# Kernel tuning notes

Measured on AMD Instinct MI355X. Metric: run time of the kernel, lower is better.

Reference implementation:

```python
import jax, jax.numpy as jnp
import numpy as np

N, E, D, C = 100000, 3200000, 256, 47


def _l2norm(x):
    n = jnp.sqrt(jnp.sum(x * x, axis=-1, keepdims=True))
    return x / jnp.maximum(n, 1e-12)


def setup_inputs() -> dict:
    key = jax.random.key(0)
    ks = jax.random.split(key, 12)
    w = lambda k, s: jax.random.normal(k, s, dtype=jnp.float32) * 0.05
    return {
        "x": jax.random.normal(ks[0], (N, D), dtype=jnp.float32),
        "src": jax.random.randint(ks[1], (E,), 0, N, dtype=jnp.int32),
        "dst": jnp.sort(jax.random.randint(ks[2], (E,), 0, N, dtype=jnp.int32)),
        "W_pre": w(ks[3], (D, D)), "b_pre": jnp.zeros((D,), jnp.float32),
        "Wl1": w(ks[4], (D, D)), "bl1": jnp.zeros((D,), jnp.float32),
        "Wr1": w(ks[5], (D, D)),
        "Wl2": w(ks[6], (D, D)), "bl2": jnp.zeros((D,), jnp.float32),
        "Wr2": w(ks[7], (D, D)),
        "W_jk": w(ks[8], (D, D)), "b_jk": jnp.zeros((D,), jnp.float32),
        "W_post": w(ks[9], (C, D)), "b_post": jnp.zeros((C,), jnp.float32),
    }


def _sage_conv(x, src, dst, Wl, bl, Wr):
    # aggr='add': m_i = sum_{j in N(i)} x_j  (SpMM as gather + segment_sum)
    m = jax.ops.segment_sum(x[src], dst, num_segments=N)
    out = m @ Wl.T + bl + x @ Wr.T  # lin_l(aggr) + lin_r(root)
    return _l2norm(out)            # SAGEConv normalize=True


def reference(x, src, dst, W_pre, b_pre, Wl1, bl1, Wr1, Wl2, bl2, Wr2,
              W_jk, b_jk, W_post, b_post):
    # pre-MLP (1 layer) + classifier activation; dropout=0, batch_norm off
    h = jax.nn.relu(x @ W_pre.T + b_pre)
    h = _l2norm(h)  # self.normalize
    # GraphSAGE, jk='last': act+dropout after every conv, then jk lin
    h = jax.nn.relu(_sage_conv(h, src, dst, Wl1, bl1, Wr1))
    h = jax.nn.relu(_sage_conv(h, src, dst, Wl2, bl2, Wr2))
    h = h @ W_jk.T + b_jk
    # post: act + post-MLP (1 layer)
    h = jax.nn.relu(h)
    h = h @ W_post.T + b_post
    return jax.nn.log_softmax(h, axis=-1)
```

## Files before the change

### kernel.cpp

```cpp
#include <hip/hip_runtime.h>
#include <stdint.h>

#define DEV __device__ __forceinline__

typedef __attribute__((ext_vector_type(8))) short bh8;
typedef __attribute__((ext_vector_type(4))) float f4;
typedef __attribute__((ext_vector_type(2))) uint32_t u32x2;
#define LDS_AS __attribute__((address_space(3)))
#define GLB_AS __attribute__((address_space(1)))

DEV unsigned short f2bf(float f) {
    union { float f; uint32_t u; } c; c.f = f;
    uint32_t u = c.u;
    uint32_t r = (u + 0x7fffu + ((u >> 16) & 1u)) >> 16;
    return (unsigned short)r;
}
DEV float bf2f(unsigned short h) {
    union { uint32_t u; float f; } c; c.u = ((uint32_t)h) << 16;
    return c.f;
}

DEV uint8_t f2fp8(float v) {
    const float vs = v * 256.f;
    union { float f; uint32_t u; } c; c.f = vs;
    const uint32_t u = c.u + 0x7ffffu + ((c.u >> 20) & 1u);
    const uint32_t f8 = (u >> 20) - 960u;
    return (vs < 0.015625f) ? (uint8_t)0 : (uint8_t)f8;
}
DEV float fp8w(uint32_t x) { union { uint32_t u; float f; } c; c.u = x; return c.f; }
DEV unsigned short fp82bf(uint32_t f) {
    return f ? (unsigned short)((f << 4) + 0x3800u) : (unsigned short)0;
}

DEV void gload16(const void* g, void* l) {
    __builtin_amdgcn_global_load_lds((const GLB_AS uint32_t*)g, (LDS_AS uint32_t*)l, 16, 0, 0);
}

__global__ __launch_bounds__(256) void prep_kernel(
    const float* __restrict__ w0, const float* __restrict__ w1, const float* __restrict__ w2,
    const float* __restrict__ w3, const float* __restrict__ w4, const float* __restrict__ w5,
    unsigned short* __restrict__ wbBase,
    const int* __restrict__ dst, int* __restrict__ rp, int N, int E) {
    const int b = blockIdx.x;
    if (b < 384) {
        const int wi = b >> 6;
        const int i = (b & 63) * 256 + threadIdx.x;
        const float* s = wi == 0 ? w0 : wi == 1 ? w1 : wi == 2 ? w2 : wi == 3 ? w3 : wi == 4 ? w4 : w5;
        const float4 v = ((const float4*)s)[i];
        ushort4 o; o.x = f2bf(v.x); o.y = f2bf(v.y); o.z = f2bf(v.z); o.w = f2bf(v.w);
        ((ushort4*)(wbBase + (size_t)wi * 65536))[i] = o;
    } else {
        const int i = (b - 384) * 256 + threadIdx.x;
        if (i <= N) {
            int lo = 0, hi = E;
            while (lo < hi) { int mid = (lo + hi) >> 1; if (dst[mid] < i) lo = mid + 1; else hi = mid; }
            rp[i] = lo;
        }
    }
}

__global__ __launch_bounds__(256) void agg_fp8_kernel(const uint32_t* __restrict__ h32,
                                                      const int* __restrict__ src,
                                                      const int* __restrict__ rp,
                                                      unsigned short* __restrict__ mout, int nNodes) {
    const int node = blockIdx.x * 4 + (threadIdx.x >> 6);
    if (node >= nNodes) return;
    const int lane = threadIdx.x & 63;
    const int beg = __builtin_amdgcn_readfirstlane(rp[node]);
    const int end = __builtin_amdgcn_readfirstlane(rp[node + 1]);
    float a0 = 0.f, a1 = 0.f, a2 = 0.f, a3 = 0.f;
    int e = beg;
    for (; e + 8 <= end; e += 8) {
        int s[8];
#pragma unroll
        for (int i = 0; i < 8; i++) s[i] = src[e + i];
        uint32_t w[8];
#pragma unroll
        for (int i = 0; i < 8; i++) w[i] = h32[(size_t)s[i] * 64 + lane];
#pragma unroll
        for (int i = 0; i < 8; i++) {
            a0 += fp8w((w[i] << 20) & 0x07f00000u);
            a1 += fp8w((w[i] << 12) & 0x07f00000u);
            a2 += fp8w((w[i] << 4)  & 0x07f00000u);
            a3 += fp8w((w[i] >> 4)  & 0x07f00000u);
        }
    }
    for (; e < end; ++e) {
        const uint32_t w = h32[(size_t)src[e] * 64 + lane];
        a0 += fp8w((w << 20) & 0x07f00000u);
        a1 += fp8w((w << 12) & 0x07f00000u);
        a2 += fp8w((w << 4)  & 0x07f00000u);
        a3 += fp8w((w >> 4)  & 0x07f00000u);
    }
    const float sc = 0x1p112f;
    u32x2 o;
    o.x = (uint32_t)f2bf(a0 * sc) | ((uint32_t)f2bf(a1 * sc) << 16);
    o.y = (uint32_t)f2bf(a2 * sc) | ((uint32_t)f2bf(a3 * sc) << 16);
    __builtin_nontemporal_store(o, (u32x2*)&mout[(size_t)node * 256 + (size_t)lane * 4]);
}

__global__ __launch_bounds__(256) void agg_kernel(const unsigned short* __restrict__ h,
                                                  const int* __restrict__ src,
                                                  const int* __restrict__ rp,
                                                  unsigned short* __restrict__ mout, int nNodes) {
    const int node = blockIdx.x * 4 + (threadIdx.x >> 6);
    if (node >= nNodes) return;
    const int lane = threadIdx.x & 63;
    const size_t fo = (size_t)lane * 4;
    const int beg = __builtin_amdgcn_readfirstlane(rp[node]);
    const int end = __builtin_amdgcn_readfirstlane(rp[node + 1]);
    float a0 = 0.f, a1 = 0.f, a2 = 0.f, a3 = 0.f;
    int e = beg;
    for (; e + 4 <= end; e += 4) {
        const int s0 = src[e], s1 = src[e+1], s2 = src[e+2], s3 = src[e+3];
        ushort4 v0 = *(const ushort4*)&h[(size_t)s0 * 256 + fo];
        ushort4 v1 = *(const ushort4*)&h[(size_t)s1 * 256 + fo];
        ushort4 v2 = *(const ushort4*)&h[(size_t)s2 * 256 + fo];
        ushort4 v3 = *(const ushort4*)&h[(size_t)s3 * 256 + fo];
        a0 += bf2f(v0.x) + bf2f(v1.x) + bf2f(v2.x) + bf2f(v3.x);
        a1 += bf2f(v0.y) + bf2f(v1.y) + bf2f(v2.y) + bf2f(v3.y);
        a2 += bf2f(v0.z) + bf2f(v1.z) + bf2f(v2.z) + bf2f(v3.z);
        a3 += bf2f(v0.w) + bf2f(v1.w) + bf2f(v2.w) + bf2f(v3.w);
    }
    for (; e < end; ++e) {
        const int s = src[e];
        ushort4 v = *(const ushort4*)&h[(size_t)s * 256 + fo];
        a0 += bf2f(v.x); a1 += bf2f(v.y); a2 += bf2f(v.z); a3 += bf2f(v.w);
    }
    ushort4 o;
    o.x = f2bf(a0); o.y = f2bf(a1); o.z = f2bf(a2); o.w = f2bf(a3);
    *(ushort4*)&mout[(size_t)node * 256 + fo] = o;
}

template <int NSEG, int EPMODE, bool OUTF8, bool A0CVT, bool A1F8>
__global__ __launch_bounds__(512) void gemm_kernel(
    const void* __restrict__ A0v, const void* __restrict__ A1v,
    const unsigned short* __restrict__ B0, const unsigned short* __restrict__ B1,
    const float* __restrict__ bias, unsigned short* __restrict__ Out,
    uint8_t* __restrict__ F8, int M) {
    __shared__ unsigned short Alds[2 * 128 * 32];
    __shared__ unsigned short Blds[2 * 256 * 32];
    __shared__ float ssq_lds[8][64];

    const int t = threadIdx.x;
    const int wid = t >> 6;
    const int lane = t & 63;
    const int wr2 = wid >> 2, wc = wid & 3;
    const int l15 = lane & 15;
    const int kh = lane >> 4;
    const int rowBase = blockIdx.x * 128;

    f4 acc[4][4];
#pragma unroll
    for (int m = 0; m < 4; m++)
#pragma unroll
        for (int n = 0; n < 4; n++) acc[m][n] = f4{0.f, 0.f, 0.f, 0.f};

    const int rA = t >> 2;
    const int sSlotA = (t & 3) ^ ((rA >> 1) & 3);
    int grA = rowBase + rA; if (grA > M - 1) grA = M - 1;
    const size_t gAoff = (size_t)grA * 256 + sSlotA * 8;
    const size_t gBoff0 = (size_t)rA * 256 + sSlotA * 8;
    const size_t gBoff1 = (size_t)(128 + rA) * 256 + sSlotA * 8;

    const int nsteps = NSEG * 8;
    float4 pa0, pa1;
    uint2 pa8;

    auto LOADA = [&](int s, int buf) {
        const int k0 = (s & 7) * 32;
        const bool seg1 = (NSEG == 2 && s >= 8);
        if (!seg1) {
            if (A0CVT) {
                const float* Af = (const float*)A0v + gAoff + k0;
                pa0 = *(const float4*)Af;
                pa1 = *(const float4*)(Af + 4);
            } else {
                gload16((const unsigned short*)A0v + gAoff + k0, &Alds[buf * 4096 + wid * 512]);
            }
        } else {
            if (A1F8) {
                pa8 = *(const uint2*)&((const uint8_t*)A1v)[gAoff + k0];
            } else {
                gload16((const unsigned short*)A1v + gAoff + k0, &Alds[buf * 4096 + wid * 512]);
            }
        }
    };
    auto LOADB = [&](int s, int buf) {
        const unsigned short* Bp = (NSEG == 2 && s >= 8) ? B1 : B0;
        const int k0 = (s & 7) * 32;
        gload16(Bp + gBoff0 + k0, &Blds[buf * 8192 + wid * 512]);
        gload16(Bp + gBoff1 + k0, &Blds[buf * 8192 + 4096 + wid * 512]);
    };
    auto WRITEA = [&](int s, int buf) {
        const bool seg1 = (NSEG == 2 && s >= 8);
        if (!seg1 && A0CVT) {
            bh8 o;
            o[0] = (short)f2bf(pa0.x); o[1] = (short)f2bf(pa0.y);
            o[2] = (short)f2bf(pa0.z); o[3] = (short)f2bf(pa0.w);
            o[4] = (short)f2bf(pa1.x); o[5] = (short)f2bf(pa1.y);
            o[6] = (short)f2bf(pa1.z); o[7] = (short)f2bf(pa1.w);
            *(bh8*)&Alds[buf * 4096 + wid * 512 + lane * 8] = o;
        } else if (seg1 && A1F8) {
            bh8 o;
            o[0] = (short)fp82bf(pa8.x & 0xffu);         o[1] = (short)fp82bf((pa8.x >> 8) & 0xffu);
            o[2] = (short)fp82bf((pa8.x >> 16) & 0xffu); o[3] = (short)fp82bf((pa8.x >> 24) & 0xffu);
            o[4] = (short)fp82bf(pa8.y & 0xffu);         o[5] = (short)fp82bf((pa8.y >> 8) & 0xffu);
            o[6] = (short)fp82bf((pa8.y >> 16) & 0xffu); o[7] = (short)fp82bf((pa8.y >> 24) & 0xffu);
            *(bh8*)&Alds[buf * 4096 + wid * 512 + lane * 8] = o;
        }
    };

    LOADA(0, 0); LOADB(0, 0); WRITEA(0, 0);
    asm volatile("s_waitcnt vmcnt(0)" ::: "memory");
    __syncthreads();

#pragma unroll 2
    for (int s = 0; s < nsteps; ++s) {
        const int cur = s & 1;
        if (s + 1 < nsteps) { LOADA(s + 1, cur ^ 1); LOADB(s + 1, cur ^ 1); }
        bh8 a[4], b[4];
#pragma unroll
        for (int m = 0; m < 4; m++) {
            const int ra = wr2 * 64 + m * 16 + l15;
            a[m] = *(const bh8*)&Alds[cur * 4096 + ra * 32 + ((kh ^ ((ra >> 1) & 3)) * 8)];
        }
#pragma unroll
        for (int n = 0; n < 4; n++) {
            const int rb = wc * 64 + n * 16 + l15;
            b[n] = *(const bh8*)&Blds[cur * 8192 + rb * 32 + ((kh ^ ((rb >> 1) & 3)) * 8)];
        }
#pragma unroll
        for (int m = 0; m < 4; m++)
#pragma unroll
            for (int n = 0; n < 4; n++)
                acc[m][n] = __builtin_amdgcn_mfma_f32_16x16x32_bf16(a[m], b[n], acc[m][n], 0, 0, 0);
        if (s + 1 < nsteps) WRITEA(s + 1, cur ^ 1);
        asm volatile("s_waitcnt vmcnt(0)" ::: "memory");
        __syncthreads();
    }

    const int cBase = wc * 64 + l15;
    float sq[4][4];
#pragma unroll
    for (int m = 0; m < 4; m++) { sq[m][0] = 0.f; sq[m][1] = 0.f; sq[m][2] = 0.f; sq[m][3] = 0.f; }
#pragma unroll
    for (int n = 0; n < 4; n++) {
        const float bv = bias[cBase + n * 16];
#pragma unroll
        for (int m = 0; m < 4; m++)
#pragma unroll
            for (int r = 0; r < 4; r++) {
                float v = acc[m][n][r] + bv;
                if (EPMODE != 1) v = fmaxf(v, 0.f);
                acc[m][n][r] = v;
                sq[m][r] += v * v;
            }
    }

    if (EPMODE != 2) {
#pragma unroll
        for (int mask = 1; mask < 16; mask <<= 1)
#pragma unroll
            for (int m = 0; m < 4; m++)
#pragma unroll
                for (int r = 0; r < 4; r++) sq[m][r] += __shfl_xor(sq[m][r], mask);
        if (l15 == 0) {
#pragma unroll
            for (int m = 0; m < 4; m++)
#pragma unroll
                for (int r = 0; r < 4; r++) ssq_lds[wid][m * 16 + kh * 4 + r] = sq[m][r];
        }
        __syncthreads();
#pragma unroll
        for (int m = 0; m < 4; m++)
#pragma unroll
            for (int r = 0; r < 4; r++) {
                const int rr = m * 16 + kh * 4 + r;
                const float s = ssq_lds[wr2 * 4 + 0][rr] + ssq_lds[wr2 * 4 + 1][rr] +
                                ssq_lds[wr2 * 4 + 2][rr] + ssq_lds[wr2 * 4 + 3][rr];
                sq[m][r] = 1.f / fmaxf(sqrtf(s), 1e-12f);
            }
    }

#pragma unroll
    for (int m = 0; m < 4; m++)
#pragma unroll
        for (int r = 0; r < 4; r++) {
            const int grow = rowBase + wr2 * 64 + m * 16 + kh * 4 + r;
            if (grow < M) {
#pragma unroll
                for (int n = 0; n < 4; n++) {
                    float v = acc[m][n][r];
                    if (EPMODE != 2) v *= sq[m][r];
                    if (EPMODE == 1) v = fmaxf(v, 0.f);
                    if (OUTF8) F8[(size_t)grow * 256 + cBase + n * 16] = f2fp8(v);
                    else       Out[(size_t)grow * 256 + cBase + n * 16] = f2bf(v);
                }
            }
        }
}

template <bool AF8>
__global__ __launch_bounds__(256) void jkfinal_kernel(
    const void* __restrict__ Av,
    const unsigned short* __restrict__ Bjk,
    const float* __restrict__ bjk,
    const float* __restrict__ Wp, const float* __restrict__ bp,
    float* __restrict__ out, int M) {
    __shared__ unsigned short S[20480];
    __shared__ unsigned short Tlds[64 * 256];

    const int t = threadIdx.x;
    const int wid = t >> 6;
    const int lane = t & 63;
    const int wc = wid;
    const int l15 = lane & 15;
    const int kh = lane >> 4;
    const int rowBase = blockIdx.x * 64;

    f4 acc[4][4];
#pragma unroll
    for (int m = 0; m < 4; m++)
#pragma unroll
        for (int n = 0; n < 4; n++) acc[m][n] = f4{0.f, 0.f, 0.f, 0.f};

    const int rA = t >> 2;
    const int sSlotA = (t & 3) ^ ((rA >> 1) & 3);
    int grA = rowBase + rA; if (grA > M - 1) grA = M - 1;
    const size_t gAoff = (size_t)grA * 256 + sSlotA * 8;
    const size_t gBoff = (size_t)rA * 256 + sSlotA * 8;

    uint2 pa8;
    auto LOADA = [&](int s, int buf) {
        const int k0 = s * 32;
        if (AF8) pa8 = *(const uint2*)&((const uint8_t*)Av)[gAoff + k0];
        else gload16((const unsigned short*)Av + gAoff + k0, &S[buf * 2048 + wid * 512]);
    };
    auto LOADB = [&](int s, int buf) {
        const int k0 = s * 32;
#pragma unroll
        for (int p = 0; p < 4; ++p)
            gload16(Bjk + (size_t)p * 16384 + gBoff + k0,
                    &S[4096 + buf * 8192 + p * 2048 + wid * 512]);
    };
    auto WRITEA = [&](int buf) {
        if (AF8) {
            bh8 o;
            o[0] = (short)fp82bf(pa8.x & 0xffu);         o[1] = (short)fp82bf((pa8.x >> 8) & 0xffu);
            o[2] = (short)fp82bf((pa8.x >> 16) & 0xffu); o[3] = (short)fp82bf((pa8.x >> 24) & 0xffu);
            o[4] = (short)fp82bf(pa8.y & 0xffu);         o[5] = (short)fp82bf((pa8.y >> 8) & 0xffu);
            o[6] = (short)fp82bf((pa8.y >> 16) & 0xffu); o[7] = (short)fp82bf((pa8.y >> 24) & 0xffu);
            *(bh8*)&S[buf * 2048 + wid * 512 + lane * 8] = o;
        }
    };

    LOADA(0, 0); LOADB(0, 0); WRITEA(0);
    asm volatile("s_waitcnt vmcnt(0)" ::: "memory");
    __syncthreads();

#pragma unroll 2
    for (int s = 0; s < 8; ++s) {
        const int cur = s & 1;
        if (s + 1 < 8) { LOADA(s + 1, cur ^ 1); LOADB(s + 1, cur ^ 1); }
        bh8 a[4], b[4];
#pragma unroll
        for (int m = 0; m < 4; m++) {
            const int ra = m * 16 + l15;
            a[m] = *(const bh8*)&S[cur * 2048 + ra * 32 + ((kh ^ ((ra >> 1) & 3)) * 8)];
        }
#pragma unroll
        for (int n = 0; n < 4; n++) {
            const int rb = wc * 64 + n * 16 + l15;
            b[n] = *(const bh8*)&S[4096 + cur * 8192 + rb * 32 + ((kh ^ ((rb >> 1) & 3)) * 8)];
        }
#pragma unroll
        for (int m = 0; m < 4; m++)
#pragma unroll
            for (int n = 0; n < 4; n++)
                acc[m][n] = __builtin_amdgcn_mfma_f32_16x16x32_bf16(a[m], b[n], acc[m][n], 0, 0, 0);
        if (s + 1 < 8) WRITEA(cur ^ 1);
        asm volatile("s_waitcnt vmcnt(0)" ::: "memory");
        __syncthreads();
    }

    const int cBase = wc * 64 + l15;
#pragma unroll
    for (int n = 0; n < 4; n++) {
        const float bv = bjk[cBase + n * 16];
        const int slot = wc * 4 + n;
#pragma unroll
        for (int m = 0; m < 4; m++)
#pragma unroll
            for (int r = 0; r < 4; r++) {
                const int row = m * 16 + kh * 4 + r;
                const float v = fmaxf(acc[m][n][r] + bv, 0.f);
                Tlds[row * 256 + (((slot ^ ((row >> 2) & 7)) << 4) | l15)] = f2bf(v);
            }
    }
    for (int i = t; i < 48 * 32; i += 256) {
        const int rb = i >> 5, slot = i & 31;
        bh8 o;
        if (rb < 47) {
#pragma unroll
            for (int j = 0; j < 8; j++) o[j] = (short)f2bf(Wp[rb * 256 + slot * 8 + j]);
        } else {
#pragma unroll
            for (int j = 0; j < 8; j++) o[j] = 0;
        }
        *(bh8*)&S[rb * 256 + ((slot ^ (rb & 7)) * 8)] = o;
    }
    __syncthreads();

    const int lrow = wid * 16 + l15;
    bh8 a2[8];
#pragma unroll
    for (int ks = 0; ks < 8; ks++) {
        const int slot = ks * 2 + (kh >> 1);
        a2[ks] = *(const bh8*)&Tlds[lrow * 256 + (((slot ^ ((lrow >> 2) & 7)) << 4) | ((kh & 1) * 8))];
    }
    f4 acc2[3];
#pragma unroll
    for (int n = 0; n < 3; n++) acc2[n] = f4{0.f, 0.f, 0.f, 0.f};
#pragma unroll
    for (int ks = 0; ks < 8; ks++)
#pragma unroll
        for (int n = 0; n < 3; n++) {
            const int rb = n * 16 + l15;
            const bh8 b = *(const bh8*)&S[rb * 256 + (((ks * 4 + kh) ^ (rb & 7)) * 8)];
            acc2[n] = __builtin_amdgcn_mfma_f32_16x16x32_bf16(a2[ks], b, acc2[n], 0, 0, 0);
        }

    const int c0 = l15, c1 = 16 + l15, c2 = 32 + l15;
    const float b0 = bp[c0], b1 = bp[c1];
    const float b2 = (l15 < 15) ? bp[c2] : 0.f;
#pragma unroll
    for (int r = 0; r < 4; r++) {
        const int grow = rowBase + wid * 16 + kh * 4 + r;
        const float x0 = acc2[0][r] + b0;
        const float x1 = acc2[1][r] + b1;
        const float x2 = (l15 < 15) ? (acc2[2][r] + b2) : -3.0e38f;
        float mx = fmaxf(fmaxf(x0, x1), x2);
#pragma unroll
        for (int msk = 1; msk < 16; msk <<= 1) mx = fmaxf(mx, __shfl_xor(mx, msk));
        float se = __expf(x0 - mx) + __expf(x1 - mx) + ((l15 < 15) ? __expf(x2 - mx) : 0.f);
#pragma unroll
        for (int msk = 1; msk < 16; msk <<= 1) se += __shfl_xor(se, msk);
        const float ls = __logf(se) + mx;
        if (grow < M) {
            float* orow = &out[(size_t)grow * 47];
            orow[c0] = x0 - ls;
            orow[c1] = x1 - ls;
            if (l15 < 15) orow[c2] = x2 - ls;
        }
    }
}

extern "C" void kernel_launch(void* const* d_in, const int* in_sizes, int n_in,
                              void* d_out, int out_size, void* d_ws, size_t ws_size,
                              hipStream_t stream) {
    const float* x      = (const float*)d_in[0];
    const int*   src    = (const int*)d_in[1];
    const int*   dst    = (const int*)d_in[2];
    const float* W_pre  = (const float*)d_in[3];
    const float* b_pre  = (const float*)d_in[4];
    const float* Wl1    = (const float*)d_in[5];
    const float* bl1    = (const float*)d_in[6];
    const float* Wr1    = (const float*)d_in[7];
    const float* Wl2    = (const float*)d_in[8];
    const float* bl2    = (const float*)d_in[9];
    const float* Wr2    = (const float*)d_in[10];
    const float* W_jk   = (const float*)d_in[11];
    const float* b_jk   = (const float*)d_in[12];
    const float* W_post = (const float*)d_in[13];
    const float* b_post = (const float*)d_in[14];

    const int N = in_sizes[0] / 256;
    const int E = in_sizes[1];

    char* ws = (char*)d_ws;
    char* ws0 = ws;
    const size_t HB = (size_t)N * 256 * 2;
    unsigned short* bufA = (unsigned short*)ws; ws += HB;
    unsigned short* bufB = (unsigned short*)ws; ws += HB;
    unsigned short* bufC = (unsigned short*)ws; ws += HB;
    unsigned short* bufD = (unsigned short*)ws; ws += HB;
    unsigned short* wbBase = (unsigned short*)ws; ws += (size_t)6 * 65536 * 2;
    int* rp = (int*)ws; ws += (size_t)(N + 1) * 4;
    uint8_t* f8A = (uint8_t*)ws; ws += (size_t)N * 256;
    uint8_t* f8B = (uint8_t*)ws; ws += (size_t)N * 256;
    const bool useFp8 = ((size_t)(ws - ws0) <= ws_size);

    const int nbr = (N + 1 + 255) / 256;
    prep_kernel<<<384 + nbr, 256, 0, stream>>>(W_pre, Wl1, Wr1, Wl2, Wr2, W_jk,
                                               wbBase, dst, rp, N, E);
    unsigned short* wb[6];
    for (int i = 0; i < 6; i++) wb[i] = wbBase + (size_t)i * 65536;

    const int gB = (N + 127) / 128;
    const int gAgg = (N + 3) / 4;
    if (useFp8) {
        gemm_kernel<1, 0, true, true, false><<<gB, 512, 0, stream>>>(x, nullptr, wb[0], nullptr, b_pre, nullptr, f8A, N);
        agg_fp8_kernel<<<gAgg, 256, 0, stream>>>((const uint32_t*)f8A, src, rp, bufC, N);
        gemm_kernel<2, 1, true, false, true><<<gB, 512, 0, stream>>>(bufC, f8A, wb[1], wb[2], bl1, nullptr, f8B, N);
        agg_fp8_kernel<<<gAgg, 256, 0, stream>>>((const uint32_t*)f8B, src, rp, bufC, N);
        gemm_kernel<2, 1, true, false, true><<<gB, 512, 0, stream>>>(bufC, f8B, wb[3], wb[4], bl2, nullptr, f8A, N);
        jkfinal_kernel<true><<<(N + 63) / 64, 256, 0, stream>>>(f8A, wb[5], b_jk, W_post, b_post,
                                                                (float*)d_out, N);
    } else {
        gemm_kernel<1, 0, false, true, false><<<gB, 512, 0, stream>>>(x, nullptr, wb[0], nullptr, b_pre, bufB, nullptr, N);
        agg_kernel<<<gAgg, 256, 0, stream>>>(bufB, src, rp, bufC, N);
        gemm_kernel<2, 1, false, false, false><<<gB, 512, 0, stream>>>(bufC, bufB, wb[1], wb[2], bl1, bufD, nullptr, N);
        agg_kernel<<<gAgg, 256, 0, stream>>>(bufD, src, rp, bufC, N);
        gemm_kernel<2, 1, false, false, false><<<gB, 512, 0, stream>>>(bufC, bufD, wb[3], wb[4], bl2, bufA, nullptr, N);
        jkfinal_kernel<false><<<(N + 63) / 64, 256, 0, stream>>>(bufA, wb[5], b_jk, W_post, b_post,
                                                                 (float*)d_out, N);
    }
}
```

Baseline: 576.4 us.

## Overlap root GEMM with neighbor aggregation in a single heterogeneous kernel

Result: slower. 652.9 us (+13.3%).

```diff
diff --git a/kernel.cpp b/kernel.cpp
--- a/kernel.cpp
+++ b/kernel.cpp
@@ -59,44 +59,130 @@
     }
 }
 
-__global__ __launch_bounds__(256) void agg_fp8_kernel(const uint32_t* __restrict__ h32,
-                                                      const int* __restrict__ src,
-                                                      const int* __restrict__ rp,
-                                                      unsigned short* __restrict__ mout, int nNodes) {
-    const int node = blockIdx.x * 4 + (threadIdx.x >> 6);
-    if (node >= nNodes) return;
-    const int lane = threadIdx.x & 63;
-    const int beg = __builtin_amdgcn_readfirstlane(rp[node]);
-    const int end = __builtin_amdgcn_readfirstlane(rp[node + 1]);
-    float a0 = 0.f, a1 = 0.f, a2 = 0.f, a3 = 0.f;
-    int e = beg;
-    for (; e + 8 <= end; e += 8) {
-        int s[8];
-#pragma unroll
-        for (int i = 0; i < 8; i++) s[i] = src[e + i];
-        uint32_t w[8];
-#pragma unroll
-        for (int i = 0; i < 8; i++) w[i] = h32[(size_t)s[i] * 64 + lane];
-#pragma unroll
-        for (int i = 0; i < 8; i++) {
-            a0 += fp8w((w[i] << 20) & 0x07f00000u);
-            a1 += fp8w((w[i] << 12) & 0x07f00000u);
-            a2 += fp8w((w[i] << 4)  & 0x07f00000u);
-            a3 += fp8w((w[i] >> 4)  & 0x07f00000u);
-        }
-    }
-    for (; e < end; ++e) {
-        const uint32_t w = h32[(size_t)src[e] * 64 + lane];
-        a0 += fp8w((w << 20) & 0x07f00000u);
-        a1 += fp8w((w << 12) & 0x07f00000u);
-        a2 += fp8w((w << 4)  & 0x07f00000u);
-        a3 += fp8w((w >> 4)  & 0x07f00000u);
-    }
-    const float sc = 0x1p112f;
-    u32x2 o;
-    o.x = (uint32_t)f2bf(a0 * sc) | ((uint32_t)f2bf(a1 * sc) << 16);
-    o.y = (uint32_t)f2bf(a2 * sc) | ((uint32_t)f2bf(a3 * sc) << 16);
-    __builtin_nontemporal_store(o, (u32x2*)&mout[(size_t)node * 256 + (size_t)lane * 4]);
+__global__ __launch_bounds__(512) void k1_kernel(
+    const uint32_t* __restrict__ h32, const int* __restrict__ src,
+    const int* __restrict__ rp, const unsigned short* __restrict__ Wr,
+    const float* __restrict__ bias, unsigned short* __restrict__ Rout,
+    unsigned short* __restrict__ mout, int gB, int N) {
+    __shared__ unsigned short Alds[2 * 128 * 32];
+    __shared__ unsigned short Blds[2 * 256 * 32];
+    const int t = threadIdx.x;
+    const int wid = t >> 6, lane = t & 63;
+    const int bid = blockIdx.x;
+
+    if (bid % 17 != 0) {
+        const int node = (bid - bid / 17 - 1) * 8 + wid;
+        if (node >= N) return;
+        const int beg = __builtin_amdgcn_readfirstlane(rp[node]);
+        const int end = __builtin_amdgcn_readfirstlane(rp[node + 1]);
+        float a0 = 0.f, a1 = 0.f, a2 = 0.f, a3 = 0.f;
+        int e = beg;
+        for (; e + 8 <= end; e += 8) {
+            int s[8];
+#pragma unroll
+            for (int i = 0; i < 8; i++) s[i] = src[e + i];
+            uint32_t w[8];
+#pragma unroll
+            for (int i = 0; i < 8; i++) w[i] = h32[(size_t)s[i] * 64 + lane];
+#pragma unroll
+            for (int i = 0; i < 8; i++) {
+                a0 += fp8w((w[i] << 20) & 0x07f00000u);
+                a1 += fp8w((w[i] << 12) & 0x07f00000u);
+                a2 += fp8w((w[i] << 4)  & 0x07f00000u);
+                a3 += fp8w((w[i] >> 4)  & 0x07f00000u);
+            }
+        }
+        for (; e < end; ++e) {
+            const uint32_t w = h32[(size_t)src[e] * 64 + lane];
+            a0 += fp8w((w << 20) & 0x07f00000u);
+            a1 += fp8w((w << 12) & 0x07f00000u);
+            a2 += fp8w((w << 4)  & 0x07f00000u);
+            a3 += fp8w((w >> 4)  & 0x07f00000u);
+        }
+        const float sc = 0x1p112f;
+        u32x2 o;
+        o.x = (uint32_t)f2bf(a0 * sc) | ((uint32_t)f2bf(a1 * sc) << 16);
+        o.y = (uint32_t)f2bf(a2 * sc) | ((uint32_t)f2bf(a3 * sc) << 16);
+        __builtin_nontemporal_store(o, (u32x2*)&mout[(size_t)node * 256 + (size_t)lane * 4]);
+        return;
+    }
+
+    const int gemmId = bid / 17;
+    const int wr2 = wid >> 2, wc = wid & 3;
+    const int l15 = lane & 15, kh = lane >> 4;
+    const int rowBase = gemmId * 128;
+
+    f4 acc[4][4];
+#pragma unroll
+    for (int m = 0; m < 4; m++)
+#pragma unroll
+        for (int n = 0; n < 4; n++) acc[m][n] = f4{0.f, 0.f, 0.f, 0.f};
+
+    const int rA = t >> 2;
+    const int sSlotA = (t & 3) ^ ((rA >> 1) & 3);
+    int grA = rowBase + rA; if (grA > N - 1) grA = N - 1;
+    const size_t gAoff = (size_t)grA * 256 + sSlotA * 8;
+    const size_t gBoff0 = (size_t)rA * 256 + sSlotA * 8;
+    const size_t gBoff1 = (size_t)(128 + rA) * 256 + sSlotA * 8;
+    const uint8_t* h8 = (const uint8_t*)h32;
+
+    uint2 pa8;
+    auto LOADA = [&](int s) { pa8 = *(const uint2*)&h8[gAoff + s * 32]; };
+    auto LOADB = [&](int s, int buf) {
+        gload16(Wr + gBoff0 + s * 32, &Blds[buf * 8192 + wid * 512]);
+        gload16(Wr + gBoff1 + s * 32, &Blds[buf * 8192 + 4096 + wid * 512]);
+    };
+    auto WRITEA = [&](int buf) {
+        bh8 o;
+        o[0] = (short)fp82bf(pa8.x & 0xffu);         o[1] = (short)fp82bf((pa8.x >> 8) & 0xffu);
+        o[2] = (short)fp82bf((pa8.x >> 16) & 0xffu); o[3] = (short)fp82bf((pa8.x >> 24) & 0xffu);
+        o[4] = (short)fp82bf(pa8.y & 0xffu);         o[5] = (short)fp82bf((pa8.y >> 8) & 0xffu);
+        o[6] = (short)fp82bf((pa8.y >> 16) & 0xffu); o[7] = (short)fp82bf((pa8.y >> 24) & 0xffu);
+        *(bh8*)&Alds[buf * 4096 + wid * 512 + lane * 8] = o;
+    };
+
+    LOADA(0); LOADB(0, 0); WRITEA(0);
+    asm volatile("s_waitcnt vmcnt(0)" ::: "memory");
+    __syncthreads();
+
+#pragma unroll 2
+    for (int s = 0; s < 8; ++s) {
+        const int cur = s & 1;
+        if (s + 1 < 8) { LOADA(s + 1); LOADB(s + 1, cur ^ 1); }
+        bh8 a[4], b[4];
+#pragma unroll
+        for (int m = 0; m < 4; m++) {
+            const int ra = wr2 * 64 + m * 16 + l15;
+            a[m] = *(const bh8*)&Alds[cur * 4096 + ra * 32 + ((kh ^ ((ra >> 1) & 3)) * 8)];
+        }
+#pragma unroll
+        for (int n = 0; n < 4; n++) {
+            const int rb = wc * 64 + n * 16 + l15;
+            b[n] = *(const bh8*)&Blds[cur * 8192 + rb * 32 + ((kh ^ ((rb >> 1) & 3)) * 8)];
+        }
+#pragma unroll
+        for (int m = 0; m < 4; m++)
+#pragma unroll
+            for (int n = 0; n < 4; n++)
+                acc[m][n] = __builtin_amdgcn_mfma_f32_16x16x32_bf16(a[m], b[n], acc[m][n], 0, 0, 0);
+        if (s + 1 < 8) WRITEA(cur ^ 1);
+        asm volatile("s_waitcnt vmcnt(0)" ::: "memory");
+        __syncthreads();
+    }
+
+    const int cBase = wc * 64 + l15;
+#pragma unroll
+    for (int n = 0; n < 4; n++) {
+        const float bv = bias[cBase + n * 16];
+#pragma unroll
+        for (int m = 0; m < 4; m++)
+#pragma unroll
+            for (int r = 0; r < 4; r++) {
+                const int grow = rowBase + wr2 * 64 + m * 16 + kh * 4 + r;
+                if (grow < N)
+                    Rout[(size_t)grow * 256 + cBase + n * 16] = f2bf(acc[m][n][r] + bv);
+            }
+    }
 }
 
 __global__ __launch_bounds__(256) void agg_kernel(const unsigned short* __restrict__ h,
@@ -132,12 +218,12 @@
     *(ushort4*)&mout[(size_t)node * 256 + fo] = o;
 }
 
-template <int NSEG, int EPMODE, bool OUTF8, bool A0CVT, bool A1F8>
+template <int NSEG, int EPMODE, bool OUTF8, bool A0CVT, bool A1F8, bool ADDR>
 __global__ __launch_bounds__(512) void gemm_kernel(
     const void* __restrict__ A0v, const void* __restrict__ A1v,
     const unsigned short* __restrict__ B0, const unsigned short* __restrict__ B1,
-    const float* __restrict__ bias, unsigned short* __restrict__ Out,
-    uint8_t* __restrict__ F8, int M) {
+    const float* __restrict__ bias, const unsigned short* __restrict__ Rm,
+    unsigned short* __restrict__ Out, uint8_t* __restrict__ F8, int M) {
     __shared__ unsigned short Alds[2 * 128 * 32];
     __shared__ unsigned short Blds[2 * 256 * 32];
     __shared__ float ssq_lds[8][64];
@@ -246,12 +332,17 @@
     for (int m = 0; m < 4; m++) { sq[m][0] = 0.f; sq[m][1] = 0.f; sq[m][2] = 0.f; sq[m][3] = 0.f; }
 #pragma unroll
     for (int n = 0; n < 4; n++) {
-        const float bv = bias[cBase + n * 16];
+        const float bv = ADDR ? 0.f : bias[cBase + n * 16];
 #pragma unroll
         for (int m = 0; m < 4; m++)
 #pragma unroll
             for (int r = 0; r < 4; r++) {
                 float v = acc[m][n][r] + bv;
+                if (ADDR) {
+                    int grow = rowBase + wr2 * 64 + m * 16 + kh * 4 + r;
+                    if (grow > M - 1) grow = M - 1;
+                    v += bf2f(Rm[(size_t)grow * 256 + cBase + n * 16]);
+                }
                 if (EPMODE != 1) v = fmaxf(v, 0.f);
                 acc[m][n][r] = v;
                 sq[m][r] += v * v;
@@ -498,21 +589,33 @@
     for (int i = 0; i < 6; i++) wb[i] = wbBase + (size_t)i * 65536;
 
     const int gB = (N + 127) / 128;
-    const int gAgg = (N + 3) / 4;
     if (useFp8) {
-        gemm_kernel<1, 0, true, true, false><<<gB, 512, 0, stream>>>(x, nullptr, wb[0], nullptr, b_pre, nullptr, f8A, N);
-        agg_fp8_kernel<<<gAgg, 256, 0, stream>>>((const uint32_t*)f8A, src, rp, bufC, N);
-        gemm_kernel<2, 1, true, false, true><<<gB, 512, 0, stream>>>(bufC, f8A, wb[1], wb[2], bl1, nullptr, f8B, N);
-        agg_fp8_kernel<<<gAgg, 256, 0, stream>>>((const uint32_t*)f8B, src, rp, bufC, N);
-        gemm_kernel<2, 1, true, false, true><<<gB, 512, 0, stream>>>(bufC, f8B, wb[3], wb[4], bl2, nullptr, f8A, N);
+        const int gAgg8 = (N + 7) / 8;
+        int L = gB * 17;
+        while (L - (L + 16) / 17 < gAgg8) L += 17;
+
+        gemm_kernel<1, 0, true, true, false, false><<<gB, 512, 0, stream>>>(
+            x, nullptr, wb[0], nullptr, b_pre, nullptr, nullptr, f8A, N);
+        k1_kernel<<<L, 512, 0, stream>>>((const uint32_t*)f8A, src, rp, wb[2], bl1,
+                                         bufD, bufC, gB, N);
+        gemm_kernel<1, 1, true, false, false, true><<<gB, 512, 0, stream>>>(
+            bufC, nullptr, wb[1], nullptr, nullptr, bufD, nullptr, f8B, N);
+        k1_kernel<<<L, 512, 0, stream>>>((const uint32_t*)f8B, src, rp, wb[4], bl2,
+                                         bufD, bufC, gB, N);
+        gemm_kernel<1, 1, true, false, false, true><<<gB, 512, 0, stream>>>(
+            bufC, nullptr, wb[3], nullptr, nullptr, bufD, nullptr, f8A, N);
         jkfinal_kernel<true><<<(N + 63) / 64, 256, 0, stream>>>(f8A, wb[5], b_jk, W_post, b_post,
                                                                 (float*)d_out, N);
     } else {
-        gemm_kernel<1, 0, false, true, false><<<gB, 512, 0, stream>>>(x, nullptr, wb[0], nullptr, b_pre, bufB, nullptr, N);
+        const int gAgg = (N + 3) / 4;
+        gemm_kernel<1, 0, false, true, false, false><<<gB, 512, 0, stream>>>(
+            x, nullptr, wb[0], nullptr, b_pre, nullptr, bufB, nullptr, N);
         agg_kernel<<<gAgg, 256, 0, stream>>>(bufB, src, rp, bufC, N);
-        gemm_kernel<2, 1, false, false, false><<<gB, 512, 0, stream>>>(bufC, bufB, wb[1], wb[2], bl1, bufD, nullptr, N);
+        gemm_kernel<2, 1, false, false, false, false><<<gB, 512, 0, stream>>>(
+            bufC, bufB, wb[1], wb[2], bl1, nullptr, bufD, nullptr, N);
         agg_kernel<<<gAgg, 256, 0, stream>>>(bufD, src, rp, bufC, N);
-        gemm_kernel<2, 1, false, false, false><<<gB, 512, 0, stream>>>(bufC, bufD, wb[3], wb[4], bl2, bufA, nullptr, N);
+        gemm_kernel<2, 1, false, false, false, false><<<gB, 512, 0, stream>>>(
+            bufC, bufD, wb[3], wb[4], bl2, nullptr, bufA, nullptr, N);
         jkfinal_kernel<false><<<(N + 63) / 64, 256, 0, stream>>>(bufA, wb[5], b_jk, W_post, b_post,
                                                                  (float*)d_out, N);
     }
```
